# Kernel optimization log

Measured on AMD Instinct MI355X. Metric: run time of the kernel, lower is better.

Reference implementation:

```python
import jax, jax.numpy as jnp
import numpy as np

H = 40  # HIDDEN_SIZE


def _gru_layer(x_tbi, Wih, Whh, bih, bhh):
    """PyTorch-convention GRU layer. x_tbi: (T, B, I). Returns (ys (T,B,H), h_T (B,H)).
    Gate order in stacked weights is (r, z, n) as in torch.nn.GRU:
      r = sigmoid(W_ir x + b_ir + W_hr h + b_hr)
      z = sigmoid(W_iz x + b_iz + W_hz h + b_hz)
      n = tanh(W_in x + b_in + r * (W_hn h + b_hn))
      h' = (1 - z) * n + z * h
    """
    # Precompute all input projections in one big GEMM: (T,B,3H)
    xg = jnp.einsum('tbi,gi->tbg', x_tbi, Wih) + bih
    B = x_tbi.shape[1]
    h0 = jnp.zeros((B, H), x_tbi.dtype)

    def step(h, xg_t):
        hg = h @ Whh.T + bhh                       # (B, 3H)
        xr, xz, xn = jnp.split(xg_t, 3, axis=-1)
        hr, hz, hn = jnp.split(hg, 3, axis=-1)
        r = jax.nn.sigmoid(xr + hr)
        z = jax.nn.sigmoid(xz + hz)
        n = jnp.tanh(xn + r * hn)
        h_new = (1.0 - z) * n + z * h
        return h_new, h_new

    hT, ys = jax.lax.scan(step, h0, xg)
    return ys, hT


def setup_inputs() -> dict:
    key = jax.random.key(0)
    ks = jax.random.split(key, 9)
    B, T, I = 4096, 256, 16
    s = 1.0 / np.sqrt(H)  # torch GRU init: U(-1/sqrt(H), 1/sqrt(H))
    u = lambda k, shape: jax.random.uniform(k, shape, jnp.float32, -s, s)
    return {
        "x": jax.random.normal(ks[0], (B, T, I), jnp.float32),
        "Wih0": u(ks[1], (3 * H, I)),
        "Whh0": u(ks[2], (3 * H, H)),
        "bih0": u(ks[3], (3 * H,)),
        "bhh0": u(ks[4], (3 * H,)),
        "Wih1": u(ks[5], (3 * H, H)),
        "Whh1": u(ks[6], (3 * H, H)),
        "bih1": u(ks[7], (3 * H,)),
        "bhh1": u(ks[8], (3 * H,)),
    }


def reference(x, Wih0, Whh0, bih0, bhh0, Wih1, Whh1, bih1, bhh1):
    # batch_first input (B,T,I) -> time-major (T,B,I) for scan
    x_tbi = jnp.transpose(x, (1, 0, 2))
    y0, _ = _gru_layer(x_tbi, Wih0, Whh0, bih0, bhh0)   # layer 0 full sequence
    _, hT = _gru_layer(y0, Wih1, Whh1, bih1, bhh1)      # layer 1 final state
    return hT  # (B, H) == h[-1]
```

## Files before the change

kernel.cpp:

```cpp
#include <hip/hip_runtime.h>

#define T_STEPS 256
#define HID 40
#define EPB 16
#define NTHR 1024
#define RR0 72
#define RR1 56
#define P0 (16 * RR0)
#define P1 (16 * RR1)
#define OL1 (2 * P0)
#define STOT (2 * P0 + 2 * P1)

typedef __attribute__((ext_vector_type(8))) short bf16x8;
typedef __attribute__((ext_vector_type(4))) float f32x4;

__device__ __forceinline__ unsigned short bf16_rne(float v) {
    unsigned int x = __float_as_uint(v);
    unsigned int r = x + 0x7FFFu + ((x >> 16) & 1u);
    return (unsigned short)(r >> 16);
}
__device__ __forceinline__ unsigned short bf16_cvt(float v) {
    unsigned int r;
    asm("v_cvt_pk_bf16_f32 %0, %1, %2" : "=v"(r) : "v"(v), "v"(v));
    return (unsigned short)r;
}
__device__ __forceinline__ float sigm(float v) {
    return __builtin_amdgcn_rcpf(1.0f + __builtin_amdgcn_exp2f(-1.4426950408889634f * v));
}
__device__ __forceinline__ float tanh_f(float v) {
    return 1.0f - 2.0f * __builtin_amdgcn_rcpf(__builtin_amdgcn_exp2f(2.8853900817779268f * v) + 1.0f);
}

#define MF(A_, B_, C_) C_ = __builtin_amdgcn_mfma_f32_16x16x32_bf16(A_, B_, C_, 0, 0, 0)
#define PINV(v) asm volatile("" : "+v"(v))

#define BAR() asm volatile("s_waitcnt lgkmcnt(0)\n\ts_barrier" ::: "memory")

__device__ bf16x8 afrag(const float* Whh, const float* Wih, int KX,
                        int rh, int rx, int c, int qrow) {
    bf16x8 f;
    #pragma unroll
    for (int j = 0; j < 8; ++j) f[j] = 0;
    #pragma unroll
    for (int j = 0; j < 8; ++j) {
        const int k = 32 * c + qrow * 8 + j;
        if (k < 40) {
            if (rh >= 0) f[j] = (short)bf16_rne(Whh[rh * 40 + k]);
        } else if (k < 40 + KX) {
            if (rx >= 0) f[j] = (short)bf16_rne(Wih[rx * KX + (k - 40)]);
        }
    }
    return f;
}

__global__ __launch_bounds__(NTHR, 4)
void gru2_kernel(const float* __restrict__ x,
                 const float* __restrict__ Wih0, const float* __restrict__ Whh0,
                 const float* __restrict__ bih0, const float* __restrict__ bhh0,
                 const float* __restrict__ Wih1, const float* __restrict__ Whh1,
                 const float* __restrict__ bih1, const float* __restrict__ bhh1,
                 float* __restrict__ out)
{
    __shared__ __align__(16) unsigned short S[STOT];

    const int tid  = threadIdx.x;
    const int wid  = tid >> 6;
    const int l    = tid & 63;
    const int col  = l & 15;
    const int qrow = l >> 4;
    const int ps   = (l & 15) & 3;
    const int pu   = (l & 15) >> 2;
    const int e0   = blockIdx.x * EPB;

    const bool isL1 = wid >= 6;
    const int  NT   = (!isL1 && wid < 4) ? 2 : 1;
    const int  TA   = isL1 ? (wid - 6) : (wid < 4 ? 2 * wid : wid + 4);
    const int  TB   = (NT == 2) ? TA + 1 : TA;
    const bool dB   = (NT != 2);

    const float* Whh = isL1 ? Whh1 : Whh0;
    const float* Wih = isL1 ? Wih1 : Wih0;
    const float* bih = isL1 ? bih1 : bih0;
    const float* bhh = isL1 ? bhh1 : bhh0;
    const int KX = isL1 ? 40 : 16;

    bf16x8 ZF;
    #pragma unroll
    for (int j = 0; j < 8; ++j) ZF[j] = 0;
    bf16x8 F00=ZF,F01=ZF,F02=ZF, F10=ZF,F11=ZF;
    f32x4 BB0, BB1;
    {
#define RRX(u, RH, RX) \
        const int RH = (ps == 2) ? -1 : (ps == 0 ? (u) : ps == 1 ? 40 + (u) : 80 + (u)); \
        const int RX = (ps == 3) ? -1 : (ps == 0 ? (u) : ps == 1 ? 40 + (u) : 80 + (u));
        {
            const int u0 = 4 * TA + pu;
            RRX(u0, rh0, rx0);
            F00 = afrag(Whh, Wih, KX, rh0, rx0, 0, qrow);
            F01 = afrag(Whh, Wih, KX, rh0, rx0, 1, qrow);
            if (isL1) F02 = afrag(Whh, Wih, KX, rh0, rx0, 2, qrow);
        }
        if (NT == 2) {
            const int u1 = 4 * TB + pu;
            RRX(u1, rh1, rx1);
            F10 = afrag(Whh, Wih, KX, rh1, rx1, 0, qrow);
            F11 = afrag(Whh, Wih, KX, rh1, rx1, 1, qrow);
        }
        const int uc0 = 4 * TA + qrow;
        const int uc1 = 4 * TB + qrow;
        BB0[0] = bih[uc0] + bhh[uc0];
        BB0[1] = bih[40 + uc0] + bhh[40 + uc0];
        BB0[2] = bih[80 + uc0];
        BB0[3] = bhh[80 + uc0];
        BB1[0] = dB ? 0.f : (bih[uc1] + bhh[uc1]);
        BB1[1] = dB ? 0.f : (bih[40 + uc1] + bhh[40 + uc1]);
        BB1[2] = dB ? 0.f : bih[80 + uc1];
        BB1[3] = dB ? 0.f : bhh[80 + uc1];
    }
    PINV(F00); PINV(F01); PINV(F02);
    PINV(F10); PINV(F11);
    PINV(BB0); PINV(BB1);

    const int rd0 = col * RR0 + 8 * qrow;
    const int rd1 = rd0 + 32;
    int g0p0, g0p1, g1p0, g1p1, g2p0, g2p1;
    {
        auto ga = [&](int g, int p) -> int {
            if (g < 5)  return OL1 + p * P1 + col * RR1 + 8 * g;
            if (g < 10) return p * P0 + col * RR0 + 8 * (g - 5);
            return p * P0 + col * RR0;
        };
        g0p0 = ga(qrow, 0);     g0p1 = ga(qrow, 1);
        g1p0 = ga(4 + qrow, 0); g1p1 = ga(4 + qrow, 1);
        g2p0 = ga(8 + qrow, 0); g2p1 = ga(8 + qrow, 1);
    }
    const int w0  = col * RR0 + 4 * TA + qrow;
    const int w0b = col * RR0 + 4 * TB + qrow;
    const int w1  = OL1 + col * RR1 + 4 * TA + qrow;
    unsigned short* Sb = &S[0];
    float hA0 = 0.f, hA1 = 0.f;

    const bool xth = tid < 256;
    const int xe = tid >> 4, xk = tid & 15;
    const int xsl = xe * RR0 + 40 + xk;
    const float* xrow = x + (size_t)(e0 + xe) * (T_STEPS * 16) + xk;

    for (int idx = tid; idx < STOT; idx += NTHR) Sb[idx] = 0;
    __syncthreads();
    float XA = 0.f, XB = 0.f, XC = 0.f, XD = 0.f;
    if (xth) {
        Sb[xsl] = bf16_cvt(xrow[0]);
        XA = xrow[16];
        XB = xrow[32];
        XC = xrow[48];
        XD = xrow[64];
    }
    __syncthreads();

#define GMATH(C, H) \
    const float r_ = sigm(C[0]); \
    const float z_ = sigm(C[1]); \
    const float n_ = tanh_f(C[2] + r_ * C[3]); \
    H = n_ + z_ * (H - n_);

#define BODY(RP, XQ) { \
    if (!isL1) { \
        if (xth && t < T_STEPS - 1) { \
            Sb[xsl + (1 - (RP)) * P0] = bf16_cvt(XQ); \
            if (t + 5 < T_STEPS) XQ = xrow[(t + 5) * 16]; \
        } \
        if (t < T_STEPS) { \
            const bf16x8 S0 = *(const bf16x8*)(Sb + rd0 + (RP) * P0); \
            const bf16x8 S1 = *(const bf16x8*)(Sb + rd1 + (RP) * P0); \
            f32x4 c0 = __builtin_amdgcn_mfma_f32_16x16x32_bf16(F00, S0, BB0, 0, 0, 0); \
            MF(F01, S1, c0); \
            { GMATH(c0, hA0); Sb[w0 + (1 - (RP)) * P0] = bf16_cvt(hA0); } \
            if (NT == 2) { \
                f32x4 c1 = __builtin_amdgcn_mfma_f32_16x16x32_bf16(F10, S0, BB1, 0, 0, 0); \
                MF(F11, S1, c1); \
                GMATH(c1, hA1); Sb[w0b + (1 - (RP)) * P0] = bf16_cvt(hA1); \
            } \
        } \
    } else { \
        const bf16x8 S0 = *(const bf16x8*)(Sb + ((RP) ? g0p1 : g0p0)); \
        const bf16x8 S1 = *(const bf16x8*)(Sb + ((RP) ? g1p1 : g1p0)); \
        const bf16x8 S2 = *(const bf16x8*)(Sb + ((RP) ? g2p1 : g2p0)); \
        f32x4 c = __builtin_amdgcn_mfma_f32_16x16x32_bf16(F00, S0, BB0, 0, 0, 0); \
        MF(F01, S1, c); MF(F02, S2, c); \
        if (t > 0) { GMATH(c, hA0); Sb[w1 + (1 - (RP)) * P1] = bf16_cvt(hA0); } \
    } \
    ++t; \
    BAR(); }

    int t = 0;
    #pragma unroll 1
    for (int it = 0; it < 64; ++it) {
        BODY(0, XA)
        BODY(1, XB)
        BODY(0, XC)
        BODY(1, XD)
    }
    BODY(0, XA)

    if (isL1) {
        out[(size_t)(e0 + col) * HID + 4 * TA + qrow] = hA0;
    }
}

extern "C" void kernel_launch(void* const* d_in, const int* in_sizes, int n_in,
                              void* d_out, int out_size, void* d_ws, size_t ws_size,
                              hipStream_t stream) {
    const float* x    = (const float*)d_in[0];
    const float* Wih0 = (const float*)d_in[1];
    const float* Whh0 = (const float*)d_in[2];
    const float* bih0 = (const float*)d_in[3];
    const float* bhh0 = (const float*)d_in[4];
    const float* Wih1 = (const float*)d_in[5];
    const float* Whh1 = (const float*)d_in[6];
    const float* bih1 = (const float*)d_in[7];
    const float* bhh1 = (const float*)d_in[8];
    float* out = (float*)d_out;

    dim3 grid(4096 / EPB), block(NTHR);
    hipLaunchKernelGGL(gru2_kernel, grid, block, 0, stream,
                       x, Wih0, Whh0, bih0, bhh0, Wih1, Whh1, bih1, bhh1, out);
}
```

Measured before the change: 202.0 us.

## Halve block to 8 waves with 2-3 hidden tiles per wave

Drops the block from 16 to 8 waves and splits both GRU layers across 4 waves each. Each wave now owns 3 or 2 of the 10 hidden-unit tiles, with per-tile weight fragments and biases held in registers. The aim is cheaper per-step barriers and more independent MFMA chains per wave for instruction-level overlap. In exchange, each wave's serial per-timestep work grows, which adds register pressure and lengthens the recurrent critical path while the grid stays at one block per CU.

```diff
diff --git a/kernel.cpp b/kernel.cpp
--- a/kernel.cpp
+++ b/kernel.cpp
@@ -3,7 +3,7 @@
 #define T_STEPS 256
 #define HID 40
 #define EPB 16
-#define NTHR 1024
+#define NTHR 512
 #define RR0 72
 #define RR1 56
 #define P0 (16 * RR0)
@@ -72,11 +72,10 @@
     const int pu   = (l & 15) >> 2;
     const int e0   = blockIdx.x * EPB;
 
-    const bool isL1 = wid >= 6;
-    const int  NT   = (!isL1 && wid < 4) ? 2 : 1;
-    const int  TA   = isL1 ? (wid - 6) : (wid < 4 ? 2 * wid : wid + 4);
-    const int  TB   = (NT == 2) ? TA + 1 : TA;
-    const bool dB   = (NT != 2);
+    const bool isL1 = wid >= 4;
+    const int  m    = wid & 3;
+    const int  NTIL = (m < 2) ? 3 : 2;
+    const int  Tb   = (m < 2) ? 3 * m : 6 + 2 * (m - 2);
 
     const float* Whh = isL1 ? Whh1 : Whh0;
     const float* Wih = isL1 ? Wih1 : Wih0;
@@ -87,39 +86,57 @@
     bf16x8 ZF;
     #pragma unroll
     for (int j = 0; j < 8; ++j) ZF[j] = 0;
-    bf16x8 F00=ZF,F01=ZF,F02=ZF, F10=ZF,F11=ZF;
-    f32x4 BB0, BB1;
+    bf16x8 FA0=ZF,FA1=ZF,FA2=ZF, FB0=ZF,FB1=ZF,FB2=ZF, FC0=ZF,FC1=ZF,FC2=ZF;
+    f32x4 BBA, BBB, BBC;
     {
 #define RRX(u, RH, RX) \
         const int RH = (ps == 2) ? -1 : (ps == 0 ? (u) : ps == 1 ? 40 + (u) : 80 + (u)); \
         const int RX = (ps == 3) ? -1 : (ps == 0 ? (u) : ps == 1 ? 40 + (u) : 80 + (u));
         {
-            const int u0 = 4 * TA + pu;
+            const int u0 = 4 * (Tb + 0) + pu;
             RRX(u0, rh0, rx0);
-            F00 = afrag(Whh, Wih, KX, rh0, rx0, 0, qrow);
-            F01 = afrag(Whh, Wih, KX, rh0, rx0, 1, qrow);
-            if (isL1) F02 = afrag(Whh, Wih, KX, rh0, rx0, 2, qrow);
-        }
-        if (NT == 2) {
-            const int u1 = 4 * TB + pu;
+            FA0 = afrag(Whh, Wih, KX, rh0, rx0, 0, qrow);
+            FA1 = afrag(Whh, Wih, KX, rh0, rx0, 1, qrow);
+            if (isL1) FA2 = afrag(Whh, Wih, KX, rh0, rx0, 2, qrow);
+        }
+        {
+            const int u1 = 4 * (Tb + 1) + pu;
             RRX(u1, rh1, rx1);
-            F10 = afrag(Whh, Wih, KX, rh1, rx1, 0, qrow);
-            F11 = afrag(Whh, Wih, KX, rh1, rx1, 1, qrow);
-        }
-        const int uc0 = 4 * TA + qrow;
-        const int uc1 = 4 * TB + qrow;
-        BB0[0] = bih[uc0] + bhh[uc0];
-        BB0[1] = bih[40 + uc0] + bhh[40 + uc0];
-        BB0[2] = bih[80 + uc0];
-        BB0[3] = bhh[80 + uc0];
-        BB1[0] = dB ? 0.f : (bih[uc1] + bhh[uc1]);
-        BB1[1] = dB ? 0.f : (bih[40 + uc1] + bhh[40 + uc1]);
-        BB1[2] = dB ? 0.f : bih[80 + uc1];
-        BB1[3] = dB ? 0.f : bhh[80 + uc1];
-    }
-    PINV(F00); PINV(F01); PINV(F02);
-    PINV(F10); PINV(F11);
-    PINV(BB0); PINV(BB1);
+            FB0 = afrag(Whh, Wih, KX, rh1, rx1, 0, qrow);
+            FB1 = afrag(Whh, Wih, KX, rh1, rx1, 1, qrow);
+            if (isL1) FB2 = afrag(Whh, Wih, KX, rh1, rx1, 2, qrow);
+        }
+        if (NTIL == 3) {
+            const int u2 = 4 * (Tb + 2) + pu;
+            RRX(u2, rh2, rx2);
+            FC0 = afrag(Whh, Wih, KX, rh2, rx2, 0, qrow);
+            FC1 = afrag(Whh, Wih, KX, rh2, rx2, 1, qrow);
+            if (isL1) FC2 = afrag(Whh, Wih, KX, rh2, rx2, 2, qrow);
+        }
+        const int ucA = 4 * (Tb + 0) + qrow;
+        const int ucB = 4 * (Tb + 1) + qrow;
+        BBA[0] = bih[ucA] + bhh[ucA];
+        BBA[1] = bih[40 + ucA] + bhh[40 + ucA];
+        BBA[2] = bih[80 + ucA];
+        BBA[3] = bhh[80 + ucA];
+        BBB[0] = bih[ucB] + bhh[ucB];
+        BBB[1] = bih[40 + ucB] + bhh[40 + ucB];
+        BBB[2] = bih[80 + ucB];
+        BBB[3] = bhh[80 + ucB];
+        if (NTIL == 3) {
+            const int ucC = 4 * (Tb + 2) + qrow;
+            BBC[0] = bih[ucC] + bhh[ucC];
+            BBC[1] = bih[40 + ucC] + bhh[40 + ucC];
+            BBC[2] = bih[80 + ucC];
+            BBC[3] = bhh[80 + ucC];
+        } else {
+            BBC[0] = BBC[1] = BBC[2] = BBC[3] = 0.f;
+        }
+    }
+    PINV(FA0); PINV(FA1); PINV(FA2);
+    PINV(FB0); PINV(FB1); PINV(FB2);
+    PINV(FC0); PINV(FC1); PINV(FC2);
+    PINV(BBA); PINV(BBB); PINV(BBC);
 
     const int rd0 = col * RR0 + 8 * qrow;
     const int rd1 = rd0 + 32;
@@ -134,11 +151,13 @@
         g1p0 = ga(4 + qrow, 0); g1p1 = ga(4 + qrow, 1);
         g2p0 = ga(8 + qrow, 0); g2p1 = ga(8 + qrow, 1);
     }
-    const int w0  = col * RR0 + 4 * TA + qrow;
-    const int w0b = col * RR0 + 4 * TB + qrow;
-    const int w1  = OL1 + col * RR1 + 4 * TA + qrow;
+    const int wbase = isL1 ? (OL1 + col * RR1) : (col * RR0);
+    const int wA = wbase + 4 * (Tb + 0) + qrow;
+    const int wB = wbase + 4 * (Tb + 1) + qrow;
+    const int wC = wbase + 4 * (Tb + 2) + qrow;
+    const int wP = isL1 ? P1 : P0;
     unsigned short* Sb = &S[0];
-    float hA0 = 0.f, hA1 = 0.f;
+    float hA = 0.f, hB = 0.f, hC = 0.f;
 
     const bool xth = tid < 256;
     const int xe = tid >> 4, xk = tid & 15;
@@ -172,22 +191,35 @@
         if (t < T_STEPS) { \
             const bf16x8 S0 = *(const bf16x8*)(Sb + rd0 + (RP) * P0); \
             const bf16x8 S1 = *(const bf16x8*)(Sb + rd1 + (RP) * P0); \
-            f32x4 c0 = __builtin_amdgcn_mfma_f32_16x16x32_bf16(F00, S0, BB0, 0, 0, 0); \
-            MF(F01, S1, c0); \
-            { GMATH(c0, hA0); Sb[w0 + (1 - (RP)) * P0] = bf16_cvt(hA0); } \
-            if (NT == 2) { \
-                f32x4 c1 = __builtin_amdgcn_mfma_f32_16x16x32_bf16(F10, S0, BB1, 0, 0, 0); \
-                MF(F11, S1, c1); \
-                GMATH(c1, hA1); Sb[w0b + (1 - (RP)) * P0] = bf16_cvt(hA1); \
+            f32x4 c0 = __builtin_amdgcn_mfma_f32_16x16x32_bf16(FA0, S0, BBA, 0, 0, 0); \
+            MF(FA1, S1, c0); \
+            { GMATH(c0, hA); Sb[wA + (1 - (RP)) * P0] = bf16_cvt(hA); } \
+            f32x4 c1 = __builtin_amdgcn_mfma_f32_16x16x32_bf16(FB0, S0, BBB, 0, 0, 0); \
+            MF(FB1, S1, c1); \
+            { GMATH(c1, hB); Sb[wB + (1 - (RP)) * P0] = bf16_cvt(hB); } \
+            if (NTIL == 3) { \
+                f32x4 c2 = __builtin_amdgcn_mfma_f32_16x16x32_bf16(FC0, S0, BBC, 0, 0, 0); \
+                MF(FC1, S1, c2); \
+                GMATH(c2, hC); Sb[wC + (1 - (RP)) * P0] = bf16_cvt(hC); \
             } \
         } \
     } else { \
         const bf16x8 S0 = *(const bf16x8*)(Sb + ((RP) ? g0p1 : g0p0)); \
         const bf16x8 S1 = *(const bf16x8*)(Sb + ((RP) ? g1p1 : g1p0)); \
         const bf16x8 S2 = *(const bf16x8*)(Sb + ((RP) ? g2p1 : g2p0)); \
-        f32x4 c = __builtin_amdgcn_mfma_f32_16x16x32_bf16(F00, S0, BB0, 0, 0, 0); \
-        MF(F01, S1, c); MF(F02, S2, c); \
-        if (t > 0) { GMATH(c, hA0); Sb[w1 + (1 - (RP)) * P1] = bf16_cvt(hA0); } \
+        f32x4 c0 = __builtin_amdgcn_mfma_f32_16x16x32_bf16(FA0, S0, BBA, 0, 0, 0); \
+        MF(FA1, S1, c0); MF(FA2, S2, c0); \
+        f32x4 c1 = __builtin_amdgcn_mfma_f32_16x16x32_bf16(FB0, S0, BBB, 0, 0, 0); \
+        MF(FB1, S1, c1); MF(FB2, S2, c1); \
+        if (t > 0) { \
+            { GMATH(c0, hA); Sb[wA + (1 - (RP)) * P1] = bf16_cvt(hA); } \
+            { GMATH(c1, hB); Sb[wB + (1 - (RP)) * P1] = bf16_cvt(hB); } \
+        } \
+        if (NTIL == 3) { \
+            f32x4 c2 = __builtin_amdgcn_mfma_f32_16x16x32_bf16(FC0, S0, BBC, 0, 0, 0); \
+            MF(FC1, S1, c2); MF(FC2, S2, c2); \
+            if (t > 0) { GMATH(c2, hC); Sb[wC + (1 - (RP)) * P1] = bf16_cvt(hC); } \
+        } \
     } \
     ++t; \
     BAR(); }
@@ -203,7 +235,10 @@
     BODY(0, XA)
 
     if (isL1) {
-        out[(size_t)(e0 + col) * HID + 4 * TA + qrow] = hA0;
+        float* op = out + (size_t)(e0 + col) * HID + 4 * Tb + qrow;
+        op[0] = hA;
+        op[4] = hB;
+        if (NTIL == 3) op[8] = hC;
     }
 }
 
```

Result: slower. 227.7 us (+12.7%).
